# Optimization experiments

Measured on AMD Instinct MI355X. Metric: run time of the kernel, lower is better.

Reference implementation:

```python
import jax, jax.numpy as jnp
import numpy as np

N, E, F_IN, HID, HEADS, NCLS = 50000, 800000, 512, 64, 4, 40
NEG_SLOPE = 0.2


def setup_inputs() -> dict:
    key = jax.random.key(0)
    ks = jax.random.split(key, 12)
    x = jax.random.normal(ks[0], (N, F_IN), jnp.float32)
    edge_index = jax.random.randint(ks[1], (2, E), 0, N, jnp.int32)
    edge_weight = jnp.ones((E,), jnp.float32)
    s1 = 1.0 / np.sqrt(F_IN)
    s2 = 1.0 / np.sqrt(HID * HEADS)
    return {
        "x": x,
        "edge_index": edge_index,
        "edge_weight": edge_weight,
        "W1": jax.random.normal(ks[2], (F_IN, HEADS * HID), jnp.float32) * s1,
        "a_src1": jax.random.normal(ks[3], (HEADS, HID), jnp.float32) * s1,
        "a_dst1": jax.random.normal(ks[4], (HEADS, HID), jnp.float32) * s1,
        "b1": jnp.zeros((HEADS * HID,), jnp.float32),
        "W2": jax.random.normal(ks[5], (HEADS * HID, NCLS), jnp.float32) * s2,
        "a_src2": jax.random.normal(ks[6], (1, NCLS), jnp.float32) * s2,
        "a_dst2": jax.random.normal(ks[7], (1, NCLS), jnp.float32) * s2,
        "b2": jnp.zeros((NCLS,), jnp.float32),
    }


def _gat_layer(x, src, dst, ew, W, a_s, a_d, b, heads, n):
    c = W.shape[1] // heads
    h = (x @ W).reshape(n, heads, c)                      # [N,H,C]
    alpha_s = jnp.einsum('nhc,hc->nh', h, a_s)            # [N,H]
    alpha_d = jnp.einsum('nhc,hc->nh', h, a_d)
    e = jax.nn.leaky_relu(alpha_s[src] + alpha_d[dst], NEG_SLOPE)  # [Et,H]
    # segment softmax over destination nodes (self-loops guarantee nonempty segs)
    m = jax.ops.segment_max(e, dst, num_segments=n)
    ex = jnp.exp(e - m[dst])
    denom = jax.ops.segment_sum(ex, dst, num_segments=n)
    alpha = ex / (denom[dst] + 1e-16)                     # [Et,H]
    alpha = alpha * ew[:, None]
    msg = h[src] * alpha[:, :, None]                      # [Et,H,C]
    out = jax.ops.segment_sum(msg, dst, num_segments=n)   # [N,H,C]
    return out.reshape(n, heads * c) + b


def reference(x, edge_index, edge_weight, W1, a_src1, a_dst1, b1, W2, a_src2, a_dst2, b2):
    n = x.shape[0]
    loop = jnp.arange(n, dtype=edge_index.dtype)
    src = jnp.concatenate([edge_index[0], loop])
    dst = jnp.concatenate([edge_index[1], loop])
    ew = jnp.concatenate([edge_weight, jnp.ones((n,), edge_weight.dtype)])
    h = _gat_layer(x, src, dst, ew, W1, a_src1, a_dst1, b1, HEADS, n)
    h = jax.nn.relu(h)  # dropout p=0.0, eval mode: no-op
    out = _gat_layer(h, src, dst, ew, W2, a_src2, a_dst2, b2, 1, n)
    return out  # Identity (log_softmax_return=False)
```

## Files before the change

kernel.cpp:

```cpp
#include <hip/hip_runtime.h>
#include <math.h>

#define N_NODES 50000
#define N_EDGES 800000
#define ET (N_EDGES + N_NODES)
#define F_IN 512
#define HID 64
#define HEADS 4
#define C1 (HEADS * HID)
#define NCLS 40
#define NEG_SLOPE 0.2f

#define BUK_SHIFT 7
#define BUK_NODES (1 << BUK_SHIFT)
#define NBUK ((N_NODES + BUK_NODES - 1) / BUK_NODES)
#define CAP 4096
#define NREP 4
#define SUBCAP (CAP / NREP)
#define BF_STRIDE 8
#define EPB_A 2048
#define NBLK_A ((ET + EPB_A - 1) / EPB_A)
#define RCAP 2560

typedef __attribute__((ext_vector_type(8))) short short8;
typedef __attribute__((ext_vector_type(4))) float floatx4;

__device__ __forceinline__ float leaky(float x) { return fmaxf(x, NEG_SLOPE * x); }

__device__ __forceinline__ unsigned short f2bf(float f) {
    unsigned u = __float_as_uint(f);
    u += 0x7fffu + ((u >> 16) & 1u);
    return (unsigned short)(u >> 16);
}
__device__ __forceinline__ float bf2f(unsigned short u) {
    return __uint_as_float(((unsigned)u) << 16);
}
__device__ __forceinline__ float bflo(unsigned v) { return __uint_as_float(v << 16); }
__device__ __forceinline__ float bfhi(unsigned v) { return __uint_as_float(v & 0xffff0000u); }

__device__ __forceinline__ void edge_sd(int e, const int* __restrict__ ei,
                                        const float* __restrict__ ew,
                                        int& s, int& d, float& w) {
    if (e < N_EDGES) { s = ei[e]; d = ei[N_EDGES + e]; w = ew[e]; }
    else             { s = d = e - N_EDGES; w = 1.f; }
}

__global__ __launch_bounds__(256) void passA_kernel(const int* __restrict__ ei,
                                                    const float* __restrict__ ew,
                                                    int* __restrict__ bfill,
                                                    int2* __restrict__ SB) {
    __shared__ int lcnt[NBUK];
    __shared__ int lbase[NBUK];
    const int t = threadIdx.x;
    const int rep = blockIdx.x & (NREP - 1);
    const int e0 = blockIdx.x * EPB_A + t;
    for (int i = t; i < NBUK; i += 256) lcnt[i] = 0;
    __syncthreads();
    int rx[8], ry[8];
    #pragma unroll
    for (int i = 0; i < 8; i++) {
        int e = e0 + i * 256;
        rx[i] = -1;
        ry[i] = 0;
        if (e < ET) {
            int s, d; float w;
            edge_sd(e, ei, ew, s, d, w);
            rx[i] = s | (d << 16);
            ry[i] = __float_as_int(w);
            atomicAdd(&lcnt[d >> BUK_SHIFT], 1);
        }
    }
    __syncthreads();
    for (int i = t; i < NBUK; i += 256) {
        int c = lcnt[i];
        lbase[i] = c ? atomicAdd(&bfill[(i * NREP + rep) * BF_STRIDE], c) : 0;
        lcnt[i] = 0;
    }
    __syncthreads();
    #pragma unroll
    for (int i = 0; i < 8; i++) {
        if (rx[i] != -1) {
            int b = ((unsigned)rx[i] >> 16) >> BUK_SHIFT;
            int r = atomicAdd(&lcnt[b], 1);
            int idx = lbase[b] + r;
            if (idx < SUBCAP)
                SB[(size_t)b * CAP + rep * SUBCAP + idx] = make_int2(rx[i], ry[i]);
        }
    }
}

__global__ __launch_bounds__(512) void scan_bbase_kernel(const int* __restrict__ bfill,
                                                         int* __restrict__ bbase) {
    __shared__ int sm[512];
    int t = threadIdx.x;
    int v = 0;
    if (t < NBUK) {
        #pragma unroll
        for (int r = 0; r < NREP; r++) {
            int c = bfill[(t * NREP + r) * BF_STRIDE];
            v += (c > SUBCAP) ? SUBCAP : c;
        }
    }
    sm[t] = v;
    __syncthreads();
    #pragma unroll
    for (int s = 1; s < 512; s <<= 1) {
        int u = (t >= s) ? sm[t - s] : 0;
        __syncthreads();
        sm[t] += u;
        __syncthreads();
    }
    if (t < NBUK) bbase[t] = sm[t] - v;
}

__global__ __launch_bounds__(512) void place_kernel(const int* __restrict__ bfill,
                                                    const int* __restrict__ bbase,
                                                    const int2* __restrict__ SB,
                                                    int* __restrict__ row_ptr,
                                                    int2* __restrict__ E2) {
    __shared__ int2 rec[RCAP];
    __shared__ int lh[BUK_NODES];
    __shared__ int excl[BUK_NODES];
    const int b = blockIdx.x;
    const int n0 = b << BUK_SHIFT;
    const int t = threadIdx.x;

    int c[NREP], off[NREP];
    int tot = 0;
    #pragma unroll
    for (int r = 0; r < NREP; r++) {
        int cc = bfill[(b * NREP + r) * BF_STRIDE];
        c[r] = (cc > SUBCAP) ? SUBCAP : cc;
        off[r] = tot;
        tot += c[r];
    }
    if (t < BUK_NODES) lh[t] = 0;
    __syncthreads();
    #pragma unroll
    for (int r = 0; r < NREP; r++) {
        const int2* base = SB + (size_t)b * CAP + r * SUBCAP;
        for (int i = t; i < c[r]; i += 512) {
            int idx = off[r] + i;
            if (idx < RCAP) rec[idx] = base[i];
        }
    }
    if (tot > RCAP) tot = RCAP;
    __syncthreads();
    for (int i = t; i < tot; i += 512)
        atomicAdd(&lh[(((unsigned)rec[i].x) >> 16) - n0], 1);
    __syncthreads();
    if (t < BUK_NODES) excl[t] = lh[t];
    __syncthreads();
    #pragma unroll
    for (int s = 1; s < BUK_NODES; s <<= 1) {
        int u = (t < BUK_NODES && t >= s) ? excl[t - s] : 0;
        __syncthreads();
        if (t < BUK_NODES) excl[t] += u;
        __syncthreads();
    }
    const int base_b = bbase[b];
    if (t < BUK_NODES) {
        int e = excl[t] - lh[t];
        int node = n0 + t;
        if (node < N_NODES) row_ptr[node] = base_b + e;
        lh[t] = e;
    }
    __syncthreads();
    for (int i = t; i < tot; i += 512) {
        int2 v = rec[i];
        int d = (((unsigned)v.x) >> 16) - n0;
        int pos = atomicAdd(&lh[d], 1);
        E2[base_b + pos] = make_int2(v.x & 0xffff, v.y);
    }
}

__global__ void wt_prep_kernel(const float* __restrict__ W, unsigned short* __restrict__ WT) {
    __shared__ float tile[32][33];
    int k0 = blockIdx.x * 32;
    int n0 = blockIdx.y * 32;
    int tx = threadIdx.x, ty = threadIdx.y;
    #pragma unroll
    for (int i = 0; i < 32; i += 8)
        tile[ty + i][tx] = W[(size_t)(k0 + ty + i) * C1 + n0 + tx];
    __syncthreads();
    #pragma unroll
    for (int i = 0; i < 32; i += 8)
        WT[(size_t)(n0 + ty + i) * F_IN + k0 + tx] = f2bf(tile[tx][ty + i]);
}

__global__ __launch_bounds__(512) void gemm1_mfma_kernel(const float* __restrict__ X,
                                                         const unsigned short* __restrict__ WT,
                                                         const float* __restrict__ a_s1,
                                                         const float* __restrict__ a_d1,
                                                         unsigned short* __restrict__ H,
                                                         float* __restrict__ AS,
                                                         float* __restrict__ AD) {
    __shared__ short As[128][40];
    __shared__ short Bs[256][40];
    const int t = threadIdx.x;
    const int m0 = blockIdx.x * 128;
    const int lane = t & 63;
    const int wave = t >> 6;
    const int wm = wave >> 2;
    const int wn = wave & 3;
    const int l15 = lane & 15;
    const int quad = lane >> 4;

    const int ar = t >> 2;
    const int ac0 = (t & 3) * 8;
    const int gr = m0 + ar;
    const int bn = t >> 1;
    const int bc0 = (t & 1) * 16;

    floatx4 acc[4][4];
    #pragma unroll
    for (int i = 0; i < 4; i++)
        #pragma unroll
        for (int j = 0; j < 4; j++) acc[i][j] = (floatx4){0.f, 0.f, 0.f, 0.f};

    for (int k0 = 0; k0 < F_IN; k0 += 32) {
        float xv[8];
        if (gr < N_NODES) {
            const float4* p = (const float4*)(X + (size_t)gr * F_IN + k0 + ac0);
            float4 v0 = p[0], v1 = p[1];
            xv[0] = v0.x; xv[1] = v0.y; xv[2] = v0.z; xv[3] = v0.w;
            xv[4] = v1.x; xv[5] = v1.y; xv[6] = v1.z; xv[7] = v1.w;
        } else {
            #pragma unroll
            for (int i = 0; i < 8; i++) xv[i] = 0.f;
        }
        short8 av;
        #pragma unroll
        for (int i = 0; i < 8; i++) av[i] = (short)f2bf(xv[i]);
        *(short8*)&As[ar][ac0] = av;

        const short8* q = (const short8*)(WT + (size_t)bn * F_IN + k0 + bc0);
        *(short8*)&Bs[bn][bc0]     = q[0];
        *(short8*)&Bs[bn][bc0 + 8] = q[1];
        __syncthreads();

        short8 a[4], b[4];
        #pragma unroll
        for (int i = 0; i < 4; i++)
            a[i] = *(const short8*)&As[wm * 64 + i * 16 + l15][quad * 8];
        #pragma unroll
        for (int j = 0; j < 4; j++)
            b[j] = *(const short8*)&Bs[wn * 64 + j * 16 + l15][quad * 8];
        #pragma unroll
        for (int i = 0; i < 4; i++)
            #pragma unroll
            for (int j = 0; j < 4; j++)
                acc[i][j] = __builtin_amdgcn_mfma_f32_16x16x32_bf16(a[i], b[j], acc[i][j], 0, 0, 0);
        __syncthreads();
    }

    float asr[4], adr[4];
    #pragma unroll
    for (int j = 0; j < 4; j++) {
        asr[j] = a_s1[wn * HID + j * 16 + l15];
        adr[j] = a_d1[wn * HID + j * 16 + l15];
    }

    #pragma unroll
    for (int i = 0; i < 4; i++) {
        int rbase = m0 + wm * 64 + i * 16 + quad * 4;
        #pragma unroll
        for (int j = 0; j < 4; j++) {
            int col = wn * 64 + j * 16 + l15;
            #pragma unroll
            for (int r = 0; r < 4; r++) {
                int row = rbase + r;
                if (row < N_NODES) H[(size_t)row * C1 + col] = f2bf(acc[i][j][r]);
            }
        }
        #pragma unroll
        for (int r = 0; r < 4; r++) {
            int row = rbase + r;
            float s_ = acc[i][0][r] * asr[0] + acc[i][1][r] * asr[1]
                     + acc[i][2][r] * asr[2] + acc[i][3][r] * asr[3];
            float d_ = acc[i][0][r] * adr[0] + acc[i][1][r] * adr[1]
                     + acc[i][2][r] * adr[2] + acc[i][3][r] * adr[3];
            #pragma unroll
            for (int m = 8; m; m >>= 1) { s_ += __shfl_xor(s_, m); d_ += __shfl_xor(d_, m); }
            if (l15 == 0 && row < N_NODES) {
                AS[row * 4 + wn] = s_;
                AD[row * 4 + wn] = d_;
            }
        }
    }
}

__global__ __launch_bounds__(256) void agg1_csr_kernel(const int* __restrict__ row_ptr,
                                                       const int2* __restrict__ E2,
                                                       const float* __restrict__ AS,
                                                       const float* __restrict__ AD,
                                                       const unsigned short* __restrict__ H,
                                                       const float* __restrict__ b1,
                                                       unsigned short* __restrict__ OUT) {
    int n = blockIdx.x * 4 + (threadIdx.x >> 6);
    int lane = threadIdx.x & 63;
    if (n >= N_NODES) return;
    int l15 = lane & 15;
    int h = lane >> 4;
    int c0 = lane * 4;
    int beg = row_ptr[n];
    int end = (n + 1 < N_NODES) ? row_ptr[n + 1] : ET;
    float ad = AD[n * 4 + h];
    float den = 0.f;
    float a0 = 0.f, a1 = 0.f, a2 = 0.f, a3 = 0.f;

    for (int base = beg; base < end; base += 16) {
        int m = end - base; if (m > 16) m = 16;
        float pw = 0.f; int s = 0;
        if (l15 < m) {
            int2 e = E2[base + l15];
            s = e.x;
            float pe = __expf(leaky(AS[e.x * 4 + h] + ad));
            den += pe;
            pw = pe * __int_as_float(e.y);
        }
        int p = 0;
        for (; p + 4 <= m; p += 4) {
            int s0 = __shfl(s, p);
            int s1 = __shfl(s, p + 1);
            int s2 = __shfl(s, p + 2);
            int s3 = __shfl(s, p + 3);
            uint2 u0 = *(const uint2*)(H + (size_t)s0 * C1 + c0);
            uint2 u1 = *(const uint2*)(H + (size_t)s1 * C1 + c0);
            uint2 u2 = *(const uint2*)(H + (size_t)s2 * C1 + c0);
            uint2 u3 = *(const uint2*)(H + (size_t)s3 * C1 + c0);
            float w0 = __shfl(pw, h * 16 + p);
            float w1 = __shfl(pw, h * 16 + p + 1);
            float w2 = __shfl(pw, h * 16 + p + 2);
            float w3 = __shfl(pw, h * 16 + p + 3);
            a0 += w0 * bflo(u0.x) + w1 * bflo(u1.x) + w2 * bflo(u2.x) + w3 * bflo(u3.x);
            a1 += w0 * bfhi(u0.x) + w1 * bfhi(u1.x) + w2 * bfhi(u2.x) + w3 * bfhi(u3.x);
            a2 += w0 * bflo(u0.y) + w1 * bflo(u1.y) + w2 * bflo(u2.y) + w3 * bflo(u3.y);
            a3 += w0 * bfhi(u0.y) + w1 * bfhi(u1.y) + w2 * bfhi(u2.y) + w3 * bfhi(u3.y);
        }
        for (; p < m; p++) {
            int s0 = __shfl(s, p);
            uint2 u0 = *(const uint2*)(H + (size_t)s0 * C1 + c0);
            float w0 = __shfl(pw, h * 16 + p);
            a0 += w0 * bflo(u0.x);
            a1 += w0 * bfhi(u0.x);
            a2 += w0 * bflo(u0.y);
            a3 += w0 * bfhi(u0.y);
        }
    }
    den += __shfl_xor(den, 1);
    den += __shfl_xor(den, 2);
    den += __shfl_xor(den, 4);
    den += __shfl_xor(den, 8);

    float r = 1.f / (den + 1e-16f);
    float4 bv = *(const float4*)(b1 + c0);
    float v0 = a0 * r + bv.x, v1 = a1 * r + bv.y, v2 = a2 * r + bv.z, v3 = a3 * r + bv.w;
    v0 = v0 > 0.f ? v0 : 0.f;
    v1 = v1 > 0.f ? v1 : 0.f;
    v2 = v2 > 0.f ? v2 : 0.f;
    v3 = v3 > 0.f ? v3 : 0.f;
    uint2 o;
    o.x = ((unsigned)f2bf(v1) << 16) | (unsigned)f2bf(v0);
    o.y = ((unsigned)f2bf(v3) << 16) | (unsigned)f2bf(v2);
    *(uint2*)(OUT + (size_t)n * C1 + c0) = o;
}

#define BROW 264
__global__ __launch_bounds__(512) void gemm2_mfma_kernel(const unsigned short* __restrict__ A,
                                                         const float* __restrict__ W2,
                                                         const float* __restrict__ a_s2,
                                                         const float* __restrict__ a_d2,
                                                         unsigned short* __restrict__ H2b,
                                                         float* __restrict__ AS2,
                                                         float* __restrict__ AD2) {
    __shared__ short As[256][40];
    __shared__ short Bs[48 * BROW];
    const int t = threadIdx.x;
    const int m0 = blockIdx.x * 256;
    const int lane = t & 63;
    const int wave = t >> 6;
    const int l15 = lane & 15;
    const int quad = lane >> 4;

    for (int i = t; i < 48 * 256; i += 512) {
        int n = i >> 8, k = i & 255;
        float v = (n < NCLS) ? W2[k * NCLS + n] : 0.f;
        Bs[n * BROW + k] = (short)f2bf(v);
    }

    const int ar = t >> 1;
    const int ac0 = (t & 1) * 16;

    floatx4 acc[2][3];
    #pragma unroll
    for (int i = 0; i < 2; i++)
        #pragma unroll
        for (int j = 0; j < 3; j++) acc[i][j] = (floatx4){0.f, 0.f, 0.f, 0.f};

    for (int k0 = 0; k0 < C1; k0 += 32) {
        const short8* q = (const short8*)(A + (size_t)(m0 + ar) * C1 + k0 + ac0);
        short8 v0 = q[0], v1 = q[1];
        __syncthreads();
        *(short8*)&As[ar][ac0]     = v0;
        *(short8*)&As[ar][ac0 + 8] = v1;
        __syncthreads();

        short8 a[2], b[3];
        #pragma unroll
        for (int i = 0; i < 2; i++)
            a[i] = *(const short8*)&As[wave * 32 + i * 16 + l15][quad * 8];
        #pragma unroll
        for (int j = 0; j < 3; j++)
            b[j] = *(const short8*)&Bs[(j * 16 + l15) * BROW + k0 + quad * 8];
        #pragma unroll
        for (int i = 0; i < 2; i++)
            #pragma unroll
            for (int j = 0; j < 3; j++)
                acc[i][j] = __builtin_amdgcn_mfma_f32_16x16x32_bf16(a[i], b[j], acc[i][j], 0, 0, 0);
    }

    float asr[3], adr[3];
    #pragma unroll
    for (int j = 0; j < 3; j++) {
        int col = j * 16 + l15;
        asr[j] = (col < NCLS) ? a_s2[col] : 0.f;
        adr[j] = (col < NCLS) ? a_d2[col] : 0.f;
    }

    #pragma unroll
    for (int i = 0; i < 2; i++) {
        #pragma unroll
        for (int r = 0; r < 4; r++) {
            int row = m0 + wave * 32 + i * 16 + quad * 4 + r;
            float s_ = acc[i][0][r] * asr[0] + acc[i][1][r] * asr[1] + acc[i][2][r] * asr[2];
            float d_ = acc[i][0][r] * adr[0] + acc[i][1][r] * adr[1] + acc[i][2][r] * adr[2];
            #pragma unroll
            for (int m = 8; m; m >>= 1) { s_ += __shfl_xor(s_, m); d_ += __shfl_xor(d_, m); }
            if (l15 == 0 && row < N_NODES) { AS2[row] = s_; AD2[row] = d_; }
            #pragma unroll
            for (int j = 0; j < 3; j++) {
                int col = j * 16 + l15;
                if (col < NCLS && row < N_NODES)
                    H2b[(size_t)row * NCLS + col] = f2bf(acc[i][j][r]);
            }
        }
    }
}

__global__ __launch_bounds__(256) void agg2_csr_kernel(const int* __restrict__ row_ptr,
                                                       const int2* __restrict__ E2,
                                                       const float* __restrict__ AS,
                                                       const float* __restrict__ AD,
                                                       const unsigned short* __restrict__ H2b,
                                                       const float* __restrict__ b2,
                                                       float* __restrict__ OUT) {
    int lane = threadIdx.x & 63;
    int n = blockIdx.x * 4 + (threadIdx.x >> 6);
    if (n >= N_NODES) return;
    int beg = row_ptr[n];
    int end = (n + 1 < N_NODES) ? row_ptr[n + 1] : ET;
    float ad = AD[n];
    bool act = lane < NCLS;
    float den = 0.f, acc = 0.f;

    for (int base = beg; base < end; base += 64) {
        int m = end - base; if (m > 64) m = 64;
        float pw = 0.f; int s = 0;
        if (lane < m) {
            int2 e = E2[base + lane];
            s = e.x;
            float pe = __expf(leaky(AS[e.x] + ad));
            den += pe;
            pw = pe * __int_as_float(e.y);
        }
        int p = 0;
        for (; p + 4 <= m; p += 4) {
            int s0 = __shfl(s, p);
            int s1 = __shfl(s, p + 1);
            int s2 = __shfl(s, p + 2);
            int s3 = __shfl(s, p + 3);
            float w0 = __shfl(pw, p);
            float w1 = __shfl(pw, p + 1);
            float w2 = __shfl(pw, p + 2);
            float w3 = __shfl(pw, p + 3);
            if (act) {
                float h0 = bf2f(H2b[(size_t)s0 * NCLS + lane]);
                float h1 = bf2f(H2b[(size_t)s1 * NCLS + lane]);
                float h2 = bf2f(H2b[(size_t)s2 * NCLS + lane]);
                float h3 = bf2f(H2b[(size_t)s3 * NCLS + lane]);
                acc += w0 * h0 + w1 * h1 + w2 * h2 + w3 * h3;
            }
        }
        for (; p < m; p++) {
            int s0 = __shfl(s, p);
            float w0 = __shfl(pw, p);
            if (act) acc += w0 * bf2f(H2b[(size_t)s0 * NCLS + lane]);
        }
    }
    den += __shfl_xor(den, 1);
    den += __shfl_xor(den, 2);
    den += __shfl_xor(den, 4);
    den += __shfl_xor(den, 8);
    den += __shfl_xor(den, 16);
    den += __shfl_xor(den, 32);
    if (act) {
        float r = 1.f / (den + 1e-16f);
        OUT[(size_t)n * NCLS + lane] = acc * r + b2[lane];
    }
}

extern "C" void kernel_launch(void* const* d_in, const int* in_sizes, int n_in,
                              void* d_out, int out_size, void* d_ws, size_t ws_size,
                              hipStream_t stream) {
    const float* x    = (const float*)d_in[0];
    const int*   ei   = (const int*)d_in[1];
    const float* ew   = (const float*)d_in[2];
    const float* W1   = (const float*)d_in[3];
    const float* a_s1 = (const float*)d_in[4];
    const float* a_d1 = (const float*)d_in[5];
    const float* b1   = (const float*)d_in[6];
    const float* W2   = (const float*)d_in[7];
    const float* a_s2 = (const float*)d_in[8];
    const float* a_d2 = (const float*)d_in[9];
    const float* b2   = (const float*)d_in[10];
    float* out = (float*)d_out;

    unsigned short* H1b  = (unsigned short*)d_ws;
    unsigned short* OUT1b = H1b + (size_t)N_NODES * C1;
    float* AS1  = (float*)(OUT1b + (size_t)N_NODES * C1);
    float* AD1  = AS1 + N_NODES * HEADS;
    int* row_ptr = (int*)(AD1 + N_NODES * HEADS);
    int* bfill = row_ptr + N_NODES;
    int* bbase = bfill + NBUK * NREP * BF_STRIDE;
    int2* E2  = (int2*)(bbase + NBUK + 1);
    unsigned short* WT = (unsigned short*)(E2 + ET);
    unsigned short* H2b = H1b;
    float* AS2  = (float*)(H2b + (size_t)N_NODES * NCLS);
    float* AD2  = AS2 + N_NODES;
    int2* SB = (int2*)H1b;

    hipMemsetAsync(bfill, 0, NBUK * NREP * BF_STRIDE * sizeof(int), stream);
    wt_prep_kernel<<<dim3(F_IN / 32, C1 / 32), dim3(32, 8), 0, stream>>>(W1, WT);
    passA_kernel<<<NBLK_A, 256, 0, stream>>>(ei, ew, bfill, SB);
    scan_bbase_kernel<<<1, 512, 0, stream>>>(bfill, bbase);
    place_kernel<<<NBUK, 512, 0, stream>>>(bfill, bbase, SB, row_ptr, E2);

    gemm1_mfma_kernel<<<(N_NODES + 127) / 128, 512, 0, stream>>>(x, WT, a_s1, a_d1, H1b, AS1, AD1);
    agg1_csr_kernel<<<(N_NODES + 3) / 4, 256, 0, stream>>>(row_ptr, E2, AS1, AD1, H1b, b1, OUT1b);

    gemm2_mfma_kernel<<<(N_NODES + 255) / 256, 512, 0, stream>>>(OUT1b, W2, a_s2, a_d2, H2b, AS2, AD2);
    agg2_csr_kernel<<<(N_NODES + 3) / 4, 256, 0, stream>>>(row_ptr, E2, AS2, AD2, H2b, b2, out);
}
```

Measured before the change: 330.1 us.

## Fuse edge bucketing into GEMM1 launch and fold bucket scan into place kernel

Edge bucketing blocks now run as extra blocks of the first-layer GEMM launch, so the compute-bound GEMM and the memory-bound edge binning run concurrently. The separate single-block scan kernel is removed; each place block computes its own base offset with a block reduction over earlier buckets' counts. SB moves to its own workspace region because it can no longer alias H1, which the GEMM writes at the same time. This removes two launches and the serialization between them, at the cost of redundant per-block reductions and extra shared memory in the fused kernel, which may lower GEMM occupancy.

Result: faster. 320.8 us (-2.8%).

```diff
diff --git a/kernel.cpp b/kernel.cpp
--- a/kernel.cpp
+++ b/kernel.cpp
@@ -20,6 +20,7 @@
 #define BF_STRIDE 8
 #define EPB_A 2048
 #define NBLK_A ((ET + EPB_A - 1) / EPB_A)
+#define NG1 ((N_NODES + 127) / 128)
 #define RCAP 2560
 
 typedef __attribute__((ext_vector_type(8))) short short8;
@@ -45,135 +46,6 @@
     else             { s = d = e - N_EDGES; w = 1.f; }
 }
 
-__global__ __launch_bounds__(256) void passA_kernel(const int* __restrict__ ei,
-                                                    const float* __restrict__ ew,
-                                                    int* __restrict__ bfill,
-                                                    int2* __restrict__ SB) {
-    __shared__ int lcnt[NBUK];
-    __shared__ int lbase[NBUK];
-    const int t = threadIdx.x;
-    const int rep = blockIdx.x & (NREP - 1);
-    const int e0 = blockIdx.x * EPB_A + t;
-    for (int i = t; i < NBUK; i += 256) lcnt[i] = 0;
-    __syncthreads();
-    int rx[8], ry[8];
-    #pragma unroll
-    for (int i = 0; i < 8; i++) {
-        int e = e0 + i * 256;
-        rx[i] = -1;
-        ry[i] = 0;
-        if (e < ET) {
-            int s, d; float w;
-            edge_sd(e, ei, ew, s, d, w);
-            rx[i] = s | (d << 16);
-            ry[i] = __float_as_int(w);
-            atomicAdd(&lcnt[d >> BUK_SHIFT], 1);
-        }
-    }
-    __syncthreads();
-    for (int i = t; i < NBUK; i += 256) {
-        int c = lcnt[i];
-        lbase[i] = c ? atomicAdd(&bfill[(i * NREP + rep) * BF_STRIDE], c) : 0;
-        lcnt[i] = 0;
-    }
-    __syncthreads();
-    #pragma unroll
-    for (int i = 0; i < 8; i++) {
-        if (rx[i] != -1) {
-            int b = ((unsigned)rx[i] >> 16) >> BUK_SHIFT;
-            int r = atomicAdd(&lcnt[b], 1);
-            int idx = lbase[b] + r;
-            if (idx < SUBCAP)
-                SB[(size_t)b * CAP + rep * SUBCAP + idx] = make_int2(rx[i], ry[i]);
-        }
-    }
-}
-
-__global__ __launch_bounds__(512) void scan_bbase_kernel(const int* __restrict__ bfill,
-                                                         int* __restrict__ bbase) {
-    __shared__ int sm[512];
-    int t = threadIdx.x;
-    int v = 0;
-    if (t < NBUK) {
-        #pragma unroll
-        for (int r = 0; r < NREP; r++) {
-            int c = bfill[(t * NREP + r) * BF_STRIDE];
-            v += (c > SUBCAP) ? SUBCAP : c;
-        }
-    }
-    sm[t] = v;
-    __syncthreads();
-    #pragma unroll
-    for (int s = 1; s < 512; s <<= 1) {
-        int u = (t >= s) ? sm[t - s] : 0;
-        __syncthreads();
-        sm[t] += u;
-        __syncthreads();
-    }
-    if (t < NBUK) bbase[t] = sm[t] - v;
-}
-
-__global__ __launch_bounds__(512) void place_kernel(const int* __restrict__ bfill,
-                                                    const int* __restrict__ bbase,
-                                                    const int2* __restrict__ SB,
-                                                    int* __restrict__ row_ptr,
-                                                    int2* __restrict__ E2) {
-    __shared__ int2 rec[RCAP];
-    __shared__ int lh[BUK_NODES];
-    __shared__ int excl[BUK_NODES];
-    const int b = blockIdx.x;
-    const int n0 = b << BUK_SHIFT;
-    const int t = threadIdx.x;
-
-    int c[NREP], off[NREP];
-    int tot = 0;
-    #pragma unroll
-    for (int r = 0; r < NREP; r++) {
-        int cc = bfill[(b * NREP + r) * BF_STRIDE];
-        c[r] = (cc > SUBCAP) ? SUBCAP : cc;
-        off[r] = tot;
-        tot += c[r];
-    }
-    if (t < BUK_NODES) lh[t] = 0;
-    __syncthreads();
-    #pragma unroll
-    for (int r = 0; r < NREP; r++) {
-        const int2* base = SB + (size_t)b * CAP + r * SUBCAP;
-        for (int i = t; i < c[r]; i += 512) {
-            int idx = off[r] + i;
-            if (idx < RCAP) rec[idx] = base[i];
-        }
-    }
-    if (tot > RCAP) tot = RCAP;
-    __syncthreads();
-    for (int i = t; i < tot; i += 512)
-        atomicAdd(&lh[(((unsigned)rec[i].x) >> 16) - n0], 1);
-    __syncthreads();
-    if (t < BUK_NODES) excl[t] = lh[t];
-    __syncthreads();
-    #pragma unroll
-    for (int s = 1; s < BUK_NODES; s <<= 1) {
-        int u = (t < BUK_NODES && t >= s) ? excl[t - s] : 0;
-        __syncthreads();
-        if (t < BUK_NODES) excl[t] += u;
-        __syncthreads();
-    }
-    const int base_b = bbase[b];
-    if (t < BUK_NODES) {
-        int e = excl[t] - lh[t];
-        int node = n0 + t;
-        if (node < N_NODES) row_ptr[node] = base_b + e;
-        lh[t] = e;
-    }
-    __syncthreads();
-    for (int i = t; i < tot; i += 512) {
-        int2 v = rec[i];
-        int d = (((unsigned)v.x) >> 16) - n0;
-        int pos = atomicAdd(&lh[d], 1);
-        E2[base_b + pos] = make_int2(v.x & 0xffff, v.y);
-    }
-}
-
 __global__ void wt_prep_kernel(const float* __restrict__ W, unsigned short* __restrict__ WT) {
     __shared__ float tile[32][33];
     int k0 = blockIdx.x * 32;
@@ -188,16 +60,63 @@
         WT[(size_t)(n0 + ty + i) * F_IN + k0 + tx] = f2bf(tile[tx][ty + i]);
 }
 
-__global__ __launch_bounds__(512) void gemm1_mfma_kernel(const float* __restrict__ X,
-                                                         const unsigned short* __restrict__ WT,
-                                                         const float* __restrict__ a_s1,
-                                                         const float* __restrict__ a_d1,
-                                                         unsigned short* __restrict__ H,
-                                                         float* __restrict__ AS,
-                                                         float* __restrict__ AD) {
+__global__ __launch_bounds__(512) void g1pa_kernel(const float* __restrict__ X,
+                                                   const unsigned short* __restrict__ WT,
+                                                   const float* __restrict__ a_s1,
+                                                   const float* __restrict__ a_d1,
+                                                   unsigned short* __restrict__ H,
+                                                   float* __restrict__ AS,
+                                                   float* __restrict__ AD,
+                                                   const int* __restrict__ ei,
+                                                   const float* __restrict__ ew,
+                                                   int* __restrict__ bfill,
+                                                   int2* __restrict__ SB) {
     __shared__ short As[128][40];
     __shared__ short Bs[256][40];
+    __shared__ int lcnt[NBUK];
+    __shared__ int lbase[NBUK];
     const int t = threadIdx.x;
+
+    if (blockIdx.x >= NG1) {
+        const int pb = blockIdx.x - NG1;
+        const int rep = pb & (NREP - 1);
+        const int e0 = pb * EPB_A + t;
+        for (int i = t; i < NBUK; i += 512) lcnt[i] = 0;
+        __syncthreads();
+        int rx[4], ry[4];
+        #pragma unroll
+        for (int i = 0; i < 4; i++) {
+            int e = e0 + i * 512;
+            rx[i] = -1;
+            ry[i] = 0;
+            if (e < ET) {
+                int s, d; float w;
+                edge_sd(e, ei, ew, s, d, w);
+                rx[i] = s | (d << 16);
+                ry[i] = __float_as_int(w);
+                atomicAdd(&lcnt[d >> BUK_SHIFT], 1);
+            }
+        }
+        __syncthreads();
+        for (int i = t; i < NBUK; i += 512) {
+            int c = lcnt[i];
+            lbase[i] = c ? atomicAdd(&bfill[(i * NREP + rep) * BF_STRIDE], c) : 0;
+            lcnt[i] = 0;
+        }
+        __syncthreads();
+        #pragma unroll
+        for (int i = 0; i < 4; i++) {
+            if (rx[i] != -1) {
+                int b = ((unsigned)rx[i] >> 16) >> BUK_SHIFT;
+                int r = atomicAdd(&lcnt[b], 1);
+                int idx = lbase[b] + r;
+                if (idx < SUBCAP)
+                    SB[(size_t)b * CAP + rep * SUBCAP + idx] = make_int2(rx[i], ry[i]);
+            }
+        }
+        return;
+    }
+
     const int m0 = blockIdx.x * 128;
     const int lane = t & 63;
     const int wave = t >> 6;
@@ -287,6 +206,82 @@
                 AD[row * 4 + wn] = d_;
             }
         }
+    }
+}
+
+__global__ __launch_bounds__(512) void place_kernel(const int* __restrict__ bfill,
+                                                    const int2* __restrict__ SB,
+                                                    int* __restrict__ row_ptr,
+                                                    int2* __restrict__ E2) {
+    __shared__ int2 rec[RCAP];
+    __shared__ int lh[BUK_NODES];
+    __shared__ int excl[BUK_NODES];
+    __shared__ int psum[512];
+    const int b = blockIdx.x;
+    const int n0 = b << BUK_SHIFT;
+    const int t = threadIdx.x;
+
+    int v = 0;
+    if (t < b) {
+        #pragma unroll
+        for (int r = 0; r < NREP; r++) {
+            int c = bfill[(t * NREP + r) * BF_STRIDE];
+            v += (c > SUBCAP) ? SUBCAP : c;
+        }
+    }
+    psum[t] = v;
+    __syncthreads();
+    for (int s = 256; s > 0; s >>= 1) {
+        if (t < s) psum[t] += psum[t + s];
+        __syncthreads();
+    }
+    const int base_b = psum[0];
+
+    int c[NREP], off[NREP];
+    int tot = 0;
+    #pragma unroll
+    for (int r = 0; r < NREP; r++) {
+        int cc = bfill[(b * NREP + r) * BF_STRIDE];
+        c[r] = (cc > SUBCAP) ? SUBCAP : cc;
+        off[r] = tot;
+        tot += c[r];
+    }
+    if (t < BUK_NODES) lh[t] = 0;
+    __syncthreads();
+    #pragma unroll
+    for (int r = 0; r < NREP; r++) {
+        const int2* base = SB + (size_t)b * CAP + r * SUBCAP;
+        for (int i = t; i < c[r]; i += 512) {
+            int idx = off[r] + i;
+            if (idx < RCAP) rec[idx] = base[i];
+        }
+    }
+    if (tot > RCAP) tot = RCAP;
+    __syncthreads();
+    for (int i = t; i < tot; i += 512)
+        atomicAdd(&lh[(((unsigned)rec[i].x) >> 16) - n0], 1);
+    __syncthreads();
+    if (t < BUK_NODES) excl[t] = lh[t];
+    __syncthreads();
+    #pragma unroll
+    for (int s = 1; s < BUK_NODES; s <<= 1) {
+        int u = (t < BUK_NODES && t >= s) ? excl[t - s] : 0;
+        __syncthreads();
+        if (t < BUK_NODES) excl[t] += u;
+        __syncthreads();
+    }
+    if (t < BUK_NODES) {
+        int e = excl[t] - lh[t];
+        int node = n0 + t;
+        if (node < N_NODES) row_ptr[node] = base_b + e;
+        lh[t] = e;
+    }
+    __syncthreads();
+    for (int i = t; i < tot; i += 512) {
+        int2 v2 = rec[i];
+        int d = (((unsigned)v2.x) >> 16) - n0;
+        int pos = atomicAdd(&lh[d], 1);
+        E2[base_b + pos] = make_int2(v2.x & 0xffff, v2.y);
     }
 }
 
@@ -532,21 +527,21 @@
     float* AD1  = AS1 + N_NODES * HEADS;
     int* row_ptr = (int*)(AD1 + N_NODES * HEADS);
     int* bfill = row_ptr + N_NODES;
-    int* bbase = bfill + NBUK * NREP * BF_STRIDE;
-    int2* E2  = (int2*)(bbase + NBUK + 1);
+    int2* E2  = (int2*)(bfill + NBUK * NREP * BF_STRIDE);
     unsigned short* WT = (unsigned short*)(E2 + ET);
+    int2* SB = (int2*)(WT + (size_t)F_IN * C1);
     unsigned short* H2b = H1b;
     float* AS2  = (float*)(H2b + (size_t)N_NODES * NCLS);
     float* AD2  = AS2 + N_NODES;
-    int2* SB = (int2*)H1b;
 
     hipMemsetAsync(bfill, 0, NBUK * NREP * BF_STRIDE * sizeof(int), stream);
     wt_prep_kernel<<<dim3(F_IN / 32, C1 / 32), dim3(32, 8), 0, stream>>>(W1, WT);
-    passA_kernel<<<NBLK_A, 256, 0, stream>>>(ei, ew, bfill, SB);
-    scan_bbase_kernel<<<1, 512, 0, stream>>>(bfill, bbase);
-    place_kernel<<<NBUK, 512, 0, stream>>>(bfill, bbase, SB, row_ptr, E2);
-
-    gemm1_mfma_kernel<<<(N_NODES + 127) / 128, 512, 0, stream>>>(x, WT, a_s1, a_d1, H1b, AS1, AD1);
+
+    g1pa_kernel<<<NG1 + NBLK_A, 512, 0, stream>>>(x, WT, a_s1, a_d1, H1b, AS1, AD1,
+                                                  ei, ew, bfill, SB);
+
+    place_kernel<<<NBUK, 512, 0, stream>>>(bfill, SB, row_ptr, E2);
+
     agg1_csr_kernel<<<(N_NODES + 3) / 4, 256, 0, stream>>>(row_ptr, E2, AS1, AD1, H1b, b1, OUT1b);
 
     gemm2_mfma_kernel<<<(N_NODES + 255) / 256, 512, 0, stream>>>(OUT1b, W2, a_s2, a_d2, H2b, AS2, AD2);
```
